# Kernel optimization log

Measured on AMD Instinct MI355X. Metric: run time of the kernel, lower is better.

The kernel has to match this reference:

```python
import jax, jax.numpy as jnp
import numpy as np

B, Q, S, C, D = 32, 128, 2048, 1024, 1024  # batch, query steps, ctx steps, ctx dim, query dim


def setup_inputs() -> dict:
    key = jax.random.key(0)
    k1, k2, k3, k4 = jax.random.split(key, 4)
    context = jax.random.normal(k1, (B, S, C), jnp.float32)
    query = jax.random.normal(k2, (Q, B, D), jnp.float32)
    context_mask = jax.random.randint(k3, (B, S), 0, 2).astype(bool)  # True = masked out
    weights = jax.random.normal(k4, (C, D), jnp.float32)  # nn.Parameter(...).normal_()
    return {"context": context, "query": query, "context_mask": context_mask, "weights": weights}


def reference(context, query, context_mask, weights):
    # Bilinear scores: (context @ W) bmm query^T -> [B, Q, S]; transposed to [Q, B, S]
    # for the per-query-step scan. temp = 1.0 so no rescaling.
    scores = jnp.einsum('bsc,cd,qbd->qbs', context, weights, query)
    neg_inf = jnp.asarray(-jnp.inf, scores.dtype)

    def step(accum, score):  # accum, score: [B, S]
        adj = jnp.where(context_mask, neg_inf, score - accum)  # coverage-adjusted score
        a = jax.nn.softmax(adj, axis=-1)
        return accum + a, a

    accum0 = jnp.zeros((B, S), scores.dtype)
    accum, attention = jax.lax.scan(step, accum0, scores)  # attention: [Q, B, S]

    # compute_composition=True branch; torch returns attention permuted to [Q, B, S],
    # accum [B, 1, S], composition [Q, B, C].
    composition = jnp.einsum('qbs,bsc->qbc', attention, context)
    return attention, accum[:, None, :], composition
```

## Files before the change

### kernel.cpp

```cpp
#include <hip/hip_runtime.h>

#define B_ 32
#define Q_ 128
#define S_ 2048
#define C_ 1024
#define D_ 1024

typedef __attribute__((ext_vector_type(8))) short bf16x8;
typedef __attribute__((ext_vector_type(4))) float f32x4;
typedef __attribute__((ext_vector_type(4))) unsigned int u32x4;

static __device__ __forceinline__ unsigned short f2bf(float f) {
  unsigned int u = __float_as_uint(f);
  u = (u + 0x7FFFu + ((u >> 16) & 1u)) >> 16;
  return (unsigned short)u;
}
static __device__ __forceinline__ float bf2f(unsigned short h) {
  return __uint_as_float(((unsigned int)h) << 16);
}

static __device__ __forceinline__ void gl_lds16(const float* g, float* l) {
  __builtin_amdgcn_global_load_lds(
      (const __attribute__((address_space(1))) unsigned int*)g,
      (__attribute__((address_space(3))) unsigned int*)l, 16, 0, 0);
}

static __device__ __forceinline__ void split8(const f32x4 x0, const f32x4 x1,
                                              bf16x8& hi, bf16x8& lo) {
  u32x4 h, l;
#pragma unroll
  for (int p = 0; p < 2; ++p) {
    const unsigned int a0 = __float_as_uint(x0[2 * p]);
    const unsigned int a1 = __float_as_uint(x0[2 * p + 1]);
    h[p] = __builtin_amdgcn_perm(a1, a0, 0x07060302u);
    const float r0 = x0[2 * p]     - __uint_as_float(a0 & 0xffff0000u);
    const float r1 = x0[2 * p + 1] - __uint_as_float(a1 & 0xffff0000u);
    l[p] = __builtin_amdgcn_perm(__float_as_uint(r1), __float_as_uint(r0), 0x07060302u);
  }
#pragma unroll
  for (int p = 0; p < 2; ++p) {
    const unsigned int a0 = __float_as_uint(x1[2 * p]);
    const unsigned int a1 = __float_as_uint(x1[2 * p + 1]);
    h[2 + p] = __builtin_amdgcn_perm(a1, a0, 0x07060302u);
    const float r0 = x1[2 * p]     - __uint_as_float(a0 & 0xffff0000u);
    const float r1 = x1[2 * p + 1] - __uint_as_float(a1 & 0xffff0000u);
    l[2 + p] = __builtin_amdgcn_perm(__float_as_uint(r1), __float_as_uint(r0), 0x07060302u);
  }
  hi = __builtin_bit_cast(bf16x8, h);
  lo = __builtin_bit_cast(bf16x8, l);
}

template <bool FUSE>
__global__ __launch_bounds__(256, 2)
void gemm_f32(const float* __restrict__ Aip, const float* __restrict__ Bip,
              float* __restrict__ outp, int K,
              long aBatch, long bBatch, long outBatch,
              long aRstride, long bRstride, long outRstride, int remapQB,
              unsigned short* __restrict__ fuseOut, long fuseRstride) {
  extern __shared__ char smem[];
  float* sA = (float*)smem;
  float* sB = sA + 8192;

  const int tid = threadIdx.x;
  const int lane = tid & 63;
  const int w = tid >> 6;
  const int wr = w >> 1;
  const int wc = w & 1;
  const int m0 = blockIdx.y * 128;
  const int n0 = blockIdx.x * 128;
  const int bz = blockIdx.z;
  const int frow = lane & 15;
  const int cc = lane >> 4;

  const float* Af = Aip + (long)bz * aBatch;
  const float* Bf = Bip + (long)bz * bBatch;

  f32x4 acc[4][4];
#pragma unroll
  for (int i = 0; i < 4; ++i)
#pragma unroll
    for (int j = 0; j < 4; ++j) acc[i][j] = (f32x4){0.f, 0.f, 0.f, 0.f};

  auto STAGE = [&](int ktt, int bufi) {
#pragma unroll
    for (int i = 0; i < 4; ++i) {
      const int rr = (w * 4 + i) * 8 + (lane >> 3);
      const int cs = (lane & 7) ^ (rr & 7);
      gl_lds16(Af + (long)(m0 + rr) * aRstride + ktt + cs * 4,
               sA + bufi * 4096 + (w * 4 + i) * 256);
    }
#pragma unroll
    for (int i = 0; i < 4; ++i) {
      const int rr = (w * 4 + i) * 8 + (lane >> 3);
      const int cs = (lane & 7) ^ (rr & 7);
      gl_lds16(Bf + (long)(n0 + rr) * bRstride + ktt + cs * 4,
               sB + bufi * 4096 + (w * 4 + i) * 256);
    }
  };

  const int nt = K >> 5;
  STAGE(0, 0);
  STAGE(32, 1);

  for (int t = 0; t < nt; ++t) {
    if (t + 1 < nt) { asm volatile("s_waitcnt vmcnt(8)" ::: "memory"); }
    else            { asm volatile("s_waitcnt vmcnt(0)" ::: "memory"); }
    __builtin_amdgcn_sched_barrier(0);
    asm volatile("s_barrier" ::: "memory");

    const float* sAb = sA + (t & 1) * 4096;
    const float* sBb = sB + (t & 1) * 4096;

    bf16x8 ah[4], al[4], bh[4], bl[4];
#pragma unroll
    for (int i = 0; i < 4; ++i) {
      const int row = wr * 64 + i * 16 + frow;
      const int c0 = ((cc * 2) ^ (row & 7)) << 2;
      const int c1 = ((cc * 2 + 1) ^ (row & 7)) << 2;
      split8(*(const f32x4*)(sAb + row * 32 + c0),
             *(const f32x4*)(sAb + row * 32 + c1), ah[i], al[i]);
    }
#pragma unroll
    for (int j = 0; j < 4; ++j) {
      const int row = wc * 64 + j * 16 + frow;
      const int c0 = ((cc * 2) ^ (row & 7)) << 2;
      const int c1 = ((cc * 2 + 1) ^ (row & 7)) << 2;
      split8(*(const f32x4*)(sBb + row * 32 + c0),
             *(const f32x4*)(sBb + row * 32 + c1), bh[j], bl[j]);
    }
#pragma unroll
    for (int i = 0; i < 4; ++i)
#pragma unroll
      for (int j = 0; j < 4; ++j) {
        acc[i][j] = __builtin_amdgcn_mfma_f32_16x16x32_bf16(ah[i], bh[j], acc[i][j], 0, 0, 0);
        acc[i][j] = __builtin_amdgcn_mfma_f32_16x16x32_bf16(ah[i], bl[j], acc[i][j], 0, 0, 0);
        acc[i][j] = __builtin_amdgcn_mfma_f32_16x16x32_bf16(al[i], bh[j], acc[i][j], 0, 0, 0);
      }

    if constexpr (FUSE) {
      const int k = lane & 31;
      const int nb = w * 32 + ((lane >> 5) << 4);
      unsigned short vals[16];
#pragma unroll
      for (int i = 0; i < 16; ++i) {
        const int row = nb + i;
        vals[i] = f2bf(sBb[row * 32 + (((k >> 2) ^ (row & 7)) << 2) + (k & 3)]);
      }
      unsigned short* dst = fuseOut + ((long)bz * K + t * 32 + k) * fuseRstride + n0 + nb;
      *(bf16x8*)(dst + 0) = *(const bf16x8*)(vals + 0);
      *(bf16x8*)(dst + 8) = *(const bf16x8*)(vals + 8);
    }

    asm volatile("s_barrier" ::: "memory");
    if (t + 2 < nt) STAGE((t + 2) * 32, t & 1);
  }

  float* out = outp + (long)bz * outBatch;
#pragma unroll
  for (int i = 0; i < 4; ++i) {
#pragma unroll
    for (int rr = 0; rr < 4; ++rr) {
      const int grow = m0 + wr * 64 + i * 16 + ((lane >> 4) << 2) + rr;
      const long orow = remapQB ? ((long)(grow & 31) * 128 + (grow >> 5)) : (long)grow;
      float* orp = out + orow * outRstride;
#pragma unroll
      for (int j = 0; j < 4; ++j) {
        const int col = n0 + wc * 64 + j * 16 + (lane & 15);
        orp[col] = acc[i][j][rr];
      }
    }
  }
}

static __device__ __forceinline__ void stage_copy(unsigned short* dst,
                                                  const unsigned short* base,
                                                  long rstride, int kt, int tid) {
  const int r = tid >> 1;
  const int sc = (tid & 1) << 5;
  const int swz = (r & 7) << 4;
  const unsigned short* s = base + (long)r * rstride + kt + sc;
  char* row = (char*)dst + r * 128;
#pragma unroll
  for (int j = 0; j < 4; ++j)
    *(bf16x8*)(row + ((sc * 2 + j * 16) ^ swz)) = *(const bf16x8*)(s + j * 8);
}

__global__ __launch_bounds__(256, 2)
void gemm_bf16(const unsigned short* __restrict__ Aip, const unsigned short* __restrict__ Bip,
               float* __restrict__ outp, int K,
               long aBatch, long bBatch, long outBatch,
               long aRstride, long bRstride, long outRstride) {
  extern __shared__ char smem[];
  unsigned short* sA = (unsigned short*)smem;
  unsigned short* sB = sA + 128 * 64;

  const int tid = threadIdx.x;
  const int lane = tid & 63;
  const int wid = tid >> 6;
  const int wr = wid >> 1;
  const int wc = wid & 1;
  const int m0 = blockIdx.y * 128;
  const int n0 = blockIdx.x * 128;
  const int bz = blockIdx.z;
  const int frow = lane & 15;

  f32x4 acc[4][4];
#pragma unroll
  for (int i = 0; i < 4; ++i)
#pragma unroll
    for (int j = 0; j < 4; ++j) acc[i][j] = (f32x4){0.f, 0.f, 0.f, 0.f};

  for (int kt = 0; kt < K; kt += 64) {
    stage_copy(sA, Aip + (long)bz * aBatch + (long)m0 * aRstride, aRstride, kt, tid);
    stage_copy(sB, Bip + (long)bz * bBatch + (long)n0 * bRstride, bRstride, kt, tid);
    __syncthreads();

#pragma unroll
    for (int kk = 0; kk < 2; ++kk) {
      const int kb = kk * 64 + ((lane >> 4) << 4);
      bf16x8 ah[4], bh[4];
#pragma unroll
      for (int i = 0; i < 4; ++i) {
        const int row = wr * 64 + i * 16 + frow;
        ah[i] = *(const bf16x8*)((const char*)sA + row * 128 + (kb ^ ((row & 7) << 4)));
      }
#pragma unroll
      for (int j = 0; j < 4; ++j) {
        const int row = wc * 64 + j * 16 + frow;
        bh[j] = *(const bf16x8*)((const char*)sB + row * 128 + (kb ^ ((row & 7) << 4)));
      }
#pragma unroll
      for (int i = 0; i < 4; ++i)
#pragma unroll
        for (int j = 0; j < 4; ++j)
          acc[i][j] = __builtin_amdgcn_mfma_f32_16x16x32_bf16(ah[i], bh[j], acc[i][j], 0, 0, 0);
    }
    __syncthreads();
  }

  float* out = outp + (long)bz * outBatch;
#pragma unroll
  for (int i = 0; i < 4; ++i) {
#pragma unroll
    for (int rr = 0; rr < 4; ++rr) {
      const int grow = m0 + wr * 64 + i * 16 + ((lane >> 4) << 2) + rr;
      float* orp = out + (long)grow * outRstride;
#pragma unroll
      for (int j = 0; j < 4; ++j) {
        const int col = n0 + wc * 64 + j * 16 + (lane & 15);
        orp[col] = acc[i][j][rr];
      }
    }
  }
}

template <int VM>
static __device__ __forceinline__ void scan_row(
    float* __restrict__ attn, unsigned short* __restrict__ attnb,
    int b, int q, int lane, int wid, int s0,
    const bool* msk, float* acc, f32x4& buf, float2 (&red)[2][8]) {
  const float L2E = 1.4426950408889634f;

  if constexpr (VM == 1)      asm volatile("s_waitcnt vmcnt(1)" ::: "memory");
  else if constexpr (VM == 3) asm volatile("s_waitcnt vmcnt(3)" ::: "memory");
  else                        asm volatile("s_waitcnt vmcnt(5)" ::: "memory");
  __builtin_amdgcn_sched_barrier(0);

  float adj[4];
#pragma unroll
  for (int j = 0; j < 4; ++j)
    adj[j] = msk[j] ? -1e30f : (buf[j] - acc[j]);

  int pr = q + 2; if (pr > Q_ - 1) pr = Q_ - 1;
  const float* pp = attn + ((long)(pr * B_ + b)) * S_ + s0;
  asm volatile("global_load_dwordx4 %0, %1, off"
               : "=&v"(buf)
               : "v"(pp), "v"(adj[0]), "v"(adj[1]), "v"(adj[2]), "v"(adj[3])
               : "memory");

  float lm = fmaxf(fmaxf(adj[0], adj[1]), fmaxf(adj[2], adj[3]));
#pragma unroll
  for (int off = 32; off > 0; off >>= 1) lm = fmaxf(lm, __shfl_xor(lm, off));

  float e[4];
#pragma unroll
  for (int j = 0; j < 4; ++j) {
    const float x = exp2f((adj[j] - lm) * L2E);
    e[j] = msk[j] ? 0.f : x;
  }

  float ls = (e[0] + e[1]) + (e[2] + e[3]);
#pragma unroll
  for (int off = 32; off > 0; off >>= 1) ls += __shfl_xor(ls, off);

  const int p = q & 1;
  if (lane == 0) red[p][wid] = make_float2(lm, ls);
  asm volatile("s_waitcnt lgkmcnt(0)\n\ts_barrier" ::: "memory");

  const float2 v0 = red[p][0], v1 = red[p][1], v2 = red[p][2], v3 = red[p][3];
  const float2 v4 = red[p][4], v5 = red[p][5], v6 = red[p][6], v7 = red[p][7];
  const float M = fmaxf(fmaxf(fmaxf(v0.x, v1.x), fmaxf(v2.x, v3.x)),
                        fmaxf(fmaxf(v4.x, v5.x), fmaxf(v6.x, v7.x)));
  const float tot = v0.y * exp2f((v0.x - M) * L2E) + v1.y * exp2f((v1.x - M) * L2E) +
                    v2.y * exp2f((v2.x - M) * L2E) + v3.y * exp2f((v3.x - M) * L2E) +
                    v4.y * exp2f((v4.x - M) * L2E) + v5.y * exp2f((v5.x - M) * L2E) +
                    v6.y * exp2f((v6.x - M) * L2E) + v7.y * exp2f((v7.x - M) * L2E);
  const float scale = exp2f((lm - M) * L2E) / tot;

  f32x4 av;
#pragma unroll
  for (int j = 0; j < 4; ++j) {
    av[j] = e[j] * scale;
    acc[j] += av[j];
  }
  *(f32x4*)(attn + ((long)(q * B_ + b)) * S_ + s0) = av;
  uint2 pk;
  pk.x = (unsigned int)f2bf(av[0]) | ((unsigned int)f2bf(av[1]) << 16);
  pk.y = (unsigned int)f2bf(av[2]) | ((unsigned int)f2bf(av[3]) << 16);
  *(uint2*)(attnb + ((long)b * Q_ + q) * S_ + s0) = pk;
}

__global__ __launch_bounds__(512)
void scan_kernel(const int* __restrict__ mask, float* __restrict__ attn,
                 float* __restrict__ accum_out, unsigned short* __restrict__ attnb) {
  const int b = blockIdx.x;
  const int tid = threadIdx.x;
  const int lane = tid & 63;
  const int wid = tid >> 6;
  const int s0 = tid * 4;

  __shared__ float2 red[2][8];

  const int4 mk = *(const int4*)(mask + (long)b * S_ + s0);
  const bool msk[4] = {mk.x != 0, mk.y != 0, mk.z != 0, mk.w != 0};
  asm volatile("" :: "v"(mk.x), "v"(mk.y), "v"(mk.z), "v"(mk.w));

  float acc[4] = {0.f, 0.f, 0.f, 0.f};

  f32x4 bufE, bufO;
  const float* p0 = attn + (long)b * S_ + s0;
  asm volatile("global_load_dwordx4 %0, %1, off" : "=&v"(bufE) : "v"(p0) : "memory");
  const float* p1 = attn + ((long)(B_ + b)) * S_ + s0;
  asm volatile("global_load_dwordx4 %0, %1, off" : "=&v"(bufO) : "v"(p1) : "memory");

  scan_row<1>(attn, attnb, b, 0, lane, wid, s0, msk, acc, bufE, red);
  scan_row<3>(attn, attnb, b, 1, lane, wid, s0, msk, acc, bufO, red);
  for (int q = 2; q < Q_; q += 2) {
    scan_row<5>(attn, attnb, b, q,     lane, wid, s0, msk, acc, bufE, red);
    scan_row<5>(attn, attnb, b, q + 1, lane, wid, s0, msk, acc, bufO, red);
  }

  f32x4 a4;
#pragma unroll
  for (int j = 0; j < 4; ++j) a4[j] = acc[j];
  *(f32x4*)(accum_out + (long)b * S_ + s0) = a4;
}

extern "C" void kernel_launch(void* const* d_in, const int* in_sizes, int n_in,
                              void* d_out, int out_size, void* d_ws, size_t ws_size,
                              hipStream_t stream) {
  const float* ctx   = (const float*)d_in[0];
  const float* query = (const float*)d_in[1];
  const int*   mask  = (const int*)d_in[2];
  const float* W     = (const float*)d_in[3];

  float* out = (float*)d_out;
  float* attn = out;
  float* accum_out = out + (size_t)Q_ * B_ * S_;
  float* comp = accum_out + (size_t)B_ * S_;

  char* ws = (char*)d_ws;
  float* qw = (float*)ws;
  unsigned short* ctxT  = (unsigned short*)(ws + (size_t)16 * 1024 * 1024);
  unsigned short* attnb = (unsigned short*)(ws + (size_t)16 * 1024 * 1024 +
                                            (size_t)B_ * C_ * S_ * 2);

  gemm_f32<false><<<dim3(C_ / 128, (Q_ * B_) / 128, 1), 256, 65536, stream>>>(
      query, W, qw, D_, 0L, 0L, 0L, (long)D_, (long)D_, (long)C_, 1, nullptr, 0L);

  gemm_f32<true><<<dim3(S_ / 128, 1, B_), 256, 65536, stream>>>(
      qw, ctx, attn, C_, (long)Q_ * C_, (long)S_ * C_, (long)S_,
      (long)C_, (long)C_, (long)B_ * S_, 0, ctxT, (long)S_);

  scan_kernel<<<B_, 512, 0, stream>>>(mask, attn, accum_out, attnb);

  gemm_bf16<<<dim3(C_ / 128, 1, B_), 256, 32768, stream>>>(
      attnb, ctxT, comp, S_, (long)Q_ * S_, (long)C_ * S_, (long)C_,
      (long)S_, (long)S_, (long)B_ * C_);
}
```

Measured before the change: 352.0 us.

## Double-buffer bf16 composition GEMM with async global-to-LDS loads

Replaces the register-staged global-to-LDS copy in the bf16 composition GEMM with direct global_load_lds transfers into a two-stage LDS ring. Tile t+2 is prefetched while tile t is consumed, using explicit vmcnt waits and raw barriers. The XOR swizzle moves to the source address so the LDS layout stays conflict-free. LDS per block doubles to 64KB, which may limit occupancy, and the hand-placed waitcnt/barrier ordering is fragile.

```diff
diff --git a/kernel.cpp b/kernel.cpp
--- a/kernel.cpp
+++ b/kernel.cpp
@@ -19,7 +19,7 @@
   return __uint_as_float(((unsigned int)h) << 16);
 }
 
-static __device__ __forceinline__ void gl_lds16(const float* g, float* l) {
+static __device__ __forceinline__ void gl_lds16(const void* g, void* l) {
   __builtin_amdgcn_global_load_lds(
       (const __attribute__((address_space(1))) unsigned int*)g,
       (__attribute__((address_space(3))) unsigned int*)l, 16, 0, 0);
@@ -172,19 +172,6 @@
   }
 }
 
-static __device__ __forceinline__ void stage_copy(unsigned short* dst,
-                                                  const unsigned short* base,
-                                                  long rstride, int kt, int tid) {
-  const int r = tid >> 1;
-  const int sc = (tid & 1) << 5;
-  const int swz = (r & 7) << 4;
-  const unsigned short* s = base + (long)r * rstride + kt + sc;
-  char* row = (char*)dst + r * 128;
-#pragma unroll
-  for (int j = 0; j < 4; ++j)
-    *(bf16x8*)(row + ((sc * 2 + j * 16) ^ swz)) = *(const bf16x8*)(s + j * 8);
-}
-
 __global__ __launch_bounds__(256, 2)
 void gemm_bf16(const unsigned short* __restrict__ Aip, const unsigned short* __restrict__ Bip,
                float* __restrict__ outp, int K,
@@ -192,17 +179,21 @@
                long aRstride, long bRstride, long outRstride) {
   extern __shared__ char smem[];
   unsigned short* sA = (unsigned short*)smem;
-  unsigned short* sB = sA + 128 * 64;
+  unsigned short* sB = sA + 16384;
 
   const int tid = threadIdx.x;
   const int lane = tid & 63;
-  const int wid = tid >> 6;
-  const int wr = wid >> 1;
-  const int wc = wid & 1;
+  const int w = tid >> 6;
+  const int wr = w >> 1;
+  const int wc = w & 1;
   const int m0 = blockIdx.y * 128;
   const int n0 = blockIdx.x * 128;
   const int bz = blockIdx.z;
   const int frow = lane & 15;
+  const int cc = lane >> 4;
+
+  const unsigned short* Ab = Aip + (long)bz * aBatch;
+  const unsigned short* Bb = Bip + (long)bz * bBatch;
 
   f32x4 acc[4][4];
 #pragma unroll
@@ -210,24 +201,50 @@
 #pragma unroll
     for (int j = 0; j < 4; ++j) acc[i][j] = (f32x4){0.f, 0.f, 0.f, 0.f};
 
-  for (int kt = 0; kt < K; kt += 64) {
-    stage_copy(sA, Aip + (long)bz * aBatch + (long)m0 * aRstride, aRstride, kt, tid);
-    stage_copy(sB, Bip + (long)bz * bBatch + (long)n0 * bRstride, bRstride, kt, tid);
-    __syncthreads();
+  auto STAGE = [&](int ktt, int bufi) {
+#pragma unroll
+    for (int i = 0; i < 4; ++i) {
+      const int rr = (w * 4 + i) * 8 + (lane >> 3);
+      const int cs = (lane & 7) ^ (rr & 7);
+      gl_lds16(Ab + (long)(m0 + rr) * aRstride + ktt + cs * 8,
+               sA + bufi * 8192 + (w * 4 + i) * 512);
+    }
+#pragma unroll
+    for (int i = 0; i < 4; ++i) {
+      const int rr = (w * 4 + i) * 8 + (lane >> 3);
+      const int cs = (lane & 7) ^ (rr & 7);
+      gl_lds16(Bb + (long)(n0 + rr) * bRstride + ktt + cs * 8,
+               sB + bufi * 8192 + (w * 4 + i) * 512);
+    }
+  };
+
+  const int nt = K >> 6;
+  STAGE(0, 0);
+  STAGE(64, 1);
+
+  for (int t = 0; t < nt; ++t) {
+    if (t + 1 < nt) { asm volatile("s_waitcnt vmcnt(8)" ::: "memory"); }
+    else            { asm volatile("s_waitcnt vmcnt(0)" ::: "memory"); }
+    __builtin_amdgcn_sched_barrier(0);
+    asm volatile("s_barrier" ::: "memory");
+
+    const unsigned short* sAb = sA + (t & 1) * 8192;
+    const unsigned short* sBb = sB + (t & 1) * 8192;
 
 #pragma unroll
     for (int kk = 0; kk < 2; ++kk) {
-      const int kb = kk * 64 + ((lane >> 4) << 4);
       bf16x8 ah[4], bh[4];
 #pragma unroll
       for (int i = 0; i < 4; ++i) {
         const int row = wr * 64 + i * 16 + frow;
-        ah[i] = *(const bf16x8*)((const char*)sA + row * 128 + (kb ^ ((row & 7) << 4)));
+        const int ch = kk * 4 + cc;
+        ah[i] = *(const bf16x8*)((const char*)sAb + row * 128 + ((ch ^ (row & 7)) << 4));
       }
 #pragma unroll
       for (int j = 0; j < 4; ++j) {
         const int row = wc * 64 + j * 16 + frow;
-        bh[j] = *(const bf16x8*)((const char*)sB + row * 128 + (kb ^ ((row & 7) << 4)));
+        const int ch = kk * 4 + cc;
+        bh[j] = *(const bf16x8*)((const char*)sBb + row * 128 + ((ch ^ (row & 7)) << 4));
       }
 #pragma unroll
       for (int i = 0; i < 4; ++i)
@@ -235,7 +252,9 @@
         for (int j = 0; j < 4; ++j)
           acc[i][j] = __builtin_amdgcn_mfma_f32_16x16x32_bf16(ah[i], bh[j], acc[i][j], 0, 0, 0);
     }
-    __syncthreads();
+
+    asm volatile("s_barrier" ::: "memory");
+    if (t + 2 < nt) STAGE((t + 2) * 64, t & 1);
   }
 
   float* out = outp + (long)bz * outBatch;
@@ -384,7 +403,7 @@
 
   scan_kernel<<<B_, 512, 0, stream>>>(mask, attn, accum_out, attnb);
 
-  gemm_bf16<<<dim3(C_ / 128, 1, B_), 256, 32768, stream>>>(
+  gemm_bf16<<<dim3(C_ / 128, 1, B_), 256, 65536, stream>>>(
       attnb, ctxT, comp, S_, (long)Q_ * S_, (long)C_ * S_, (long)C_,
       (long)S_, (long)S_, (long)B_ * C_);
 }
```

Result: faster. 338.1 us (-4.0%).
